# Performance work log

Measured on AMD Instinct MI355X. Metric: run time of the kernel, lower is better.

## Reference

```python
import jax, jax.numpy as jnp
import numpy as np

D_IN = 256
H = 512


def _linear_params(key, fan_in, fan_out):
    kw, kb = jax.random.split(key)
    bound = 1.0 / np.sqrt(fan_in)
    W = jax.random.uniform(kw, (fan_in, fan_out), minval=-bound, maxval=bound, dtype=jnp.float32)
    b = jax.random.uniform(kb, (fan_out,), minval=-bound, maxval=bound, dtype=jnp.float32)
    return W, b


def setup_inputs() -> dict:
    key = jax.random.key(0)
    ks = jax.random.split(key, 7)
    brick_vectors = jax.random.normal(ks[0], (8, 128, D_IN), dtype=jnp.float32)
    Wa, ba = _linear_params(ks[1], D_IN, H)
    Wb, bb = _linear_params(ks[2], H, H)
    Wca, bca = _linear_params(ks[3], 2 * H, H)
    Wcb, bcb = _linear_params(ks[4], H, H)
    Wcc, bcc = _linear_params(ks[5], H, H)
    Wo, bo = _linear_params(ks[6], H, 2)
    return {
        "brick_vectors": brick_vectors,
        "Wa": Wa, "ba": ba,
        "Wb": Wb, "bb": bb,
        "Wca": Wca, "bca": bca,
        "Wcb": Wcb, "bcb": bcb,
        "Wcc": Wcc, "bcc": bcc,
        "Wo": Wo, "bo": bo,
    }


def reference(brick_vectors, Wa, ba, Wb, bb, Wca, bca, Wcb, bcb, Wcc, bcc, Wo, bo):
    B, N, _ = brick_vectors.shape
    x = brick_vectors.reshape(-1, D_IN)            # [B*N, D_IN]
    f = jax.nn.relu(x @ Wa + ba)                   # node MLP
    f = jax.nn.relu(f @ Wb + bb)                   # [B*N, 512]
    f = f.reshape(B, N, H)
    # pairwise broadcast-concat: pair (i, j) gets cat(f[:, j], f[:, i])
    fa = jnp.broadcast_to(f[:, None, :, :], (B, N, N, H))   # varies over j (last pair axis)
    fb = jnp.broadcast_to(f[:, :, None, :], (B, N, N, H))   # varies over i
    e = jnp.concatenate((fa, fb), axis=-1).reshape(-1, 2 * H)  # [B*N*N, 1024]
    e = jax.nn.relu(e @ Wca + bca)
    e = jax.nn.relu(e @ Wcb + bcb)
    e = jax.nn.relu(e @ Wcc + bcc)
    out = e @ Wo + bo                               # [B*N*N, 2]
    return out.reshape(B, N, N, 2)
```

## Files before the change

### kernel.cpp

```cpp
#include <hip/hip_runtime.h>

typedef __bf16 bf16x8 __attribute__((ext_vector_type(8)));
typedef float f32x16 __attribute__((ext_vector_type(16)));

#define GLOAD_LDS16(gsrc, ldst)                                                   \
  __builtin_amdgcn_global_load_lds(                                               \
      (const __attribute__((address_space(1))) void*)(gsrc),                      \
      (__attribute__((address_space(3))) void*)(ldst), 16, 0, 0)

__device__ __forceinline__ void pack_one(const float* __restrict__ src,
                                         __bf16* __restrict__ dst,
                                         int t, int kbshift) {
  int e = t & 7, l = (t >> 3) & 63;
  int kb = (t >> 9) & ((1 << kbshift) - 1);
  int c = t >> (9 + kbshift);
  int k = kb * 16 + ((l >> 5) << 3) + e;
  int n = (c << 5) + (l & 31);
  dst[t] = (__bf16)src[k * 512 + n];
}

__global__ __launch_bounds__(256) void pack_all(
    const float* __restrict__ Wcb, const float* __restrict__ Wcc,
    const float* __restrict__ Wb, const float* __restrict__ Wca,
    const float* __restrict__ Wa,
    __bf16* __restrict__ Pb, __bf16* __restrict__ Pc,
    __bf16* __restrict__ PWb, __bf16* __restrict__ PH0,
    __bf16* __restrict__ PH1, __bf16* __restrict__ PWa) {
  int idx = blockIdx.x * 256 + threadIdx.x;
  if (idx < 262144) {
    pack_one(Wcb, Pb, idx, 5);
  } else if (idx < 524288) {
    pack_one(Wcc, Pc, idx - 262144, 5);
  } else if (idx < 786432) {
    pack_one(Wb, PWb, idx - 524288, 5);
  } else if (idx < 1048576) {
    pack_one(Wca, PH0, idx - 786432, 5);
  } else if (idx < 1310720) {
    pack_one(Wca + 512 * 512, PH1, idx - 1048576, 5);
  } else if (idx < 1441792) {
    pack_one(Wa, PWa, idx - 1310720, 4);
  }
}

template <int K>
__global__ __launch_bounds__(512, 2) void node_mfma(
    const float* __restrict__ A, const bf16x8* __restrict__ P0,
    const bf16x8* __restrict__ P1, const float* __restrict__ bias,
    int do_relu, float* __restrict__ C0, float* __restrict__ C1) {
  constexpr int KB = K / 16;
  constexpr int KH = K / 2;
  __shared__ __align__(16) char sA[64 * K * 2];

  int row0 = blockIdx.x * 64;
  const bf16x8* P = blockIdx.y ? P1 : P0;
  float* C = blockIdx.y ? C1 : C0;
  int tid = threadIdx.x, lane = tid & 63, w = tid >> 6;

  {
    int k2 = tid & (KH - 1);
    int rof = tid / KH;
    constexpr int RPI = 512 / KH;
#pragma unroll 4
    for (int it = 0; it < 64 / RPI; it++) {
      int r = it * RPI + rof;
      float2 aa = *(const float2*)(A + (row0 + r) * K + 2 * k2);
      unsigned short s0 = __builtin_bit_cast(unsigned short, (__bf16)aa.x);
      unsigned short s1 = __builtin_bit_cast(unsigned short, (__bf16)aa.y);
      unsigned int pk = ((unsigned int)s1 << 16) | (unsigned int)s0;
      int wbyte = r * (2 * K) + ((4 * k2) ^ ((r & 15) << 4));
      *(unsigned int*)(sA + wbyte) = pk;
    }
  }
  __syncthreads();

  int mrow = (w & 1) * 32;
  int n0 = (w >> 1) * 128;
  int cg4 = (w >> 1) * 4;
  int arow = mrow + (lane & 31);
  int sAk = (arow & 15) << 4;
  int klo = (lane >> 5) * 8;

  const bf16x8* B0 = P + ((cg4 + 0) * KB) * 64 + lane;
  const bf16x8* B1 = P + ((cg4 + 1) * KB) * 64 + lane;
  const bf16x8* B2 = P + ((cg4 + 2) * KB) * 64 + lane;
  const bf16x8* B3 = P + ((cg4 + 3) * KB) * 64 + lane;

  f32x16 acc[4];
#pragma unroll
  for (int nb = 0; nb < 4; nb++)
#pragma unroll
    for (int r = 0; r < 16; r++) acc[nb][r] = 0.f;

#pragma unroll 2
  for (int kb = 0; kb < KB; kb++) {
    int abyte = arow * (2 * K) + (((kb * 16 + klo) * 2) ^ sAk);
    bf16x8 a = *(const bf16x8*)(sA + abyte);
    bf16x8 b0 = B0[kb * 64];
    bf16x8 b1 = B1[kb * 64];
    bf16x8 b2 = B2[kb * 64];
    bf16x8 b3 = B3[kb * 64];
    acc[0] = __builtin_amdgcn_mfma_f32_32x32x16_bf16(a, b0, acc[0], 0, 0, 0);
    acc[1] = __builtin_amdgcn_mfma_f32_32x32x16_bf16(a, b1, acc[1], 0, 0, 0);
    acc[2] = __builtin_amdgcn_mfma_f32_32x32x16_bf16(a, b2, acc[2], 0, 0, 0);
    acc[3] = __builtin_amdgcn_mfma_f32_32x32x16_bf16(a, b3, acc[3], 0, 0, 0);
  }

#pragma unroll
  for (int nb = 0; nb < 4; nb++) {
    int cn = n0 + nb * 32 + (lane & 31);
    float bv = bias ? bias[cn] : 0.f;
#pragma unroll
    for (int r = 0; r < 16; r++) {
      int rr = mrow + (r & 3) + 8 * (r >> 2) + 4 * (lane >> 5);
      float val = acc[nb][r] + bv;
      if (do_relu) val = fmaxf(val, 0.f);
      C[(row0 + rr) * 512 + cn] = val;
    }
  }
}

__global__ __launch_bounds__(512, 2) void edge_kernel(
    const float* __restrict__ u, const float* __restrict__ v,
    const bf16x8* __restrict__ Pb, const bf16x8* __restrict__ Pc,
    const float* __restrict__ bca, const float* __restrict__ bcb,
    const float* __restrict__ bcc, const float* __restrict__ Wo,
    const float* __restrict__ bo, float* __restrict__ out) {
  __shared__ __align__(16) char h_raw[163840];
  char* Bst = h_raw + 131072;

  int wg = blockIdx.x;
  int i = wg & 127, b = wg >> 7;
  int tid = threadIdx.x, lane = tid & 63, w = tid >> 6;

  int mrow = (w & 1) * 32;
  int n0 = (w >> 1) * 128;
  int cg4 = (w >> 1) * 4;
  int arow = mrow + (lane & 31);
  int sA = (arow & 15) << 4;
  int klo = (lane >> 5) * 8;
  int cb0 = 2 * w;

#define STAGE_B(P, kb, sel)                                                       \
  {                                                                               \
    const char* _g0 = (const char*)((P) + (cb0 * 32 + (kb)) * 64) + lane * 16;    \
    const char* _g1 = (const char*)((P) + ((cb0 + 1) * 32 + (kb)) * 64) + lane * 16; \
    GLOAD_LDS16(_g0, Bst + (sel) * 16384 + cb0 * 1024);                           \
    GLOAD_LDS16(_g1, Bst + (sel) * 16384 + (cb0 + 1) * 1024);                     \
  }

  STAGE_B(Pb, 0, 0)

  {
    int k2 = tid & 255;
    float2 vv = *(const float2*)(v + (b * 128 + i) * 512 + 2 * k2);
    float2 bc = *(const float2*)(bca + 2 * k2);
    float vb0 = vv.x + bc.x, vb1 = vv.y + bc.y;
    const float* ub = u + (b * 128) * 512;
#pragma unroll 4
    for (int it = 0; it < 64; it++) {
      int r = it * 2 + (tid >> 8);
      float2 uu = *(const float2*)(ub + r * 512 + 2 * k2);
      float x0 = fmaxf(uu.x + vb0, 0.f);
      float x1 = fmaxf(uu.y + vb1, 0.f);
      unsigned short s0 = __builtin_bit_cast(unsigned short, (__bf16)x0);
      unsigned short s1 = __builtin_bit_cast(unsigned short, (__bf16)x1);
      unsigned int pk = ((unsigned int)s1 << 16) | (unsigned int)s0;
      int rt = r & 63;
      int wbyte = ((r >> 6) << 16) + rt * 1024 + ((4 * k2) ^ ((rt & 15) << 4));
      *(unsigned int*)(h_raw + wbyte) = pk;
    }
  }
  __syncthreads();

  f32x16 acc0[4], acc1[4];

#pragma unroll
  for (int nb = 0; nb < 4; nb++)
#pragma unroll
    for (int r = 0; r < 16; r++) { acc0[nb][r] = 0.f; acc1[nb][r] = 0.f; }
#pragma unroll 2
  for (int kb = 0; kb < 32; kb++) {
    int sel = kb & 1;
    if (kb < 31) STAGE_B(Pb, kb + 1, sel ^ 1)
    const char* bb = Bst + sel * 16384 + lane * 16;
    bf16x8 b0 = *(const bf16x8*)(bb + (cg4 + 0) * 1024);
    bf16x8 b1 = *(const bf16x8*)(bb + (cg4 + 1) * 1024);
    bf16x8 b2 = *(const bf16x8*)(bb + (cg4 + 2) * 1024);
    bf16x8 b3 = *(const bf16x8*)(bb + (cg4 + 3) * 1024);
    int abyte = arow * 1024 + (((kb * 16 + klo) * 2) ^ sA);
    bf16x8 a0 = *(const bf16x8*)(h_raw + abyte);
    bf16x8 a1 = *(const bf16x8*)(h_raw + 65536 + abyte);
    acc0[0] = __builtin_amdgcn_mfma_f32_32x32x16_bf16(a0, b0, acc0[0], 0, 0, 0);
    acc1[0] = __builtin_amdgcn_mfma_f32_32x32x16_bf16(a1, b0, acc1[0], 0, 0, 0);
    acc0[1] = __builtin_amdgcn_mfma_f32_32x32x16_bf16(a0, b1, acc0[1], 0, 0, 0);
    acc1[1] = __builtin_amdgcn_mfma_f32_32x32x16_bf16(a1, b1, acc1[1], 0, 0, 0);
    acc0[2] = __builtin_amdgcn_mfma_f32_32x32x16_bf16(a0, b2, acc0[2], 0, 0, 0);
    acc1[2] = __builtin_amdgcn_mfma_f32_32x32x16_bf16(a1, b2, acc1[2], 0, 0, 0);
    acc0[3] = __builtin_amdgcn_mfma_f32_32x32x16_bf16(a0, b3, acc0[3], 0, 0, 0);
    acc1[3] = __builtin_amdgcn_mfma_f32_32x32x16_bf16(a1, b3, acc1[3], 0, 0, 0);
    __syncthreads();
  }
  STAGE_B(Pc, 0, 0)

#pragma unroll
  for (int nb = 0; nb < 4; nb++) {
    int cn = n0 + nb * 32 + (lane & 31);
    float bbv = bcb[cn];
#pragma unroll
    for (int r = 0; r < 16; r++) {
      int row = mrow + (r & 3) + 8 * (r >> 2) + 4 * (lane >> 5);
      int byte_ = row * 1024 + ((cn * 2) ^ ((row & 15) << 4));
      *(__bf16*)(h_raw + byte_) = (__bf16)fmaxf(acc0[nb][r] + bbv, 0.f);
      *(__bf16*)(h_raw + 65536 + byte_) = (__bf16)fmaxf(acc1[nb][r] + bbv, 0.f);
    }
  }
  __syncthreads();

#pragma unroll
  for (int nb = 0; nb < 4; nb++)
#pragma unroll
    for (int r = 0; r < 16; r++) { acc0[nb][r] = 0.f; acc1[nb][r] = 0.f; }
#pragma unroll 2
  for (int kb = 0; kb < 32; kb++) {
    int sel = kb & 1;
    if (kb < 31) STAGE_B(Pc, kb + 1, sel ^ 1)
    const char* bb = Bst + sel * 16384 + lane * 16;
    bf16x8 b0 = *(const bf16x8*)(bb + (cg4 + 0) * 1024);
    bf16x8 b1 = *(const bf16x8*)(bb + (cg4 + 1) * 1024);
    bf16x8 b2 = *(const bf16x8*)(bb + (cg4 + 2) * 1024);
    bf16x8 b3 = *(const bf16x8*)(bb + (cg4 + 3) * 1024);
    int abyte = arow * 1024 + (((kb * 16 + klo) * 2) ^ sA);
    bf16x8 a0 = *(const bf16x8*)(h_raw + abyte);
    bf16x8 a1 = *(const bf16x8*)(h_raw + 65536 + abyte);
    acc0[0] = __builtin_amdgcn_mfma_f32_32x32x16_bf16(a0, b0, acc0[0], 0, 0, 0);
    acc1[0] = __builtin_amdgcn_mfma_f32_32x32x16_bf16(a1, b0, acc1[0], 0, 0, 0);
    acc0[1] = __builtin_amdgcn_mfma_f32_32x32x16_bf16(a0, b1, acc0[1], 0, 0, 0);
    acc1[1] = __builtin_amdgcn_mfma_f32_32x32x16_bf16(a1, b1, acc1[1], 0, 0, 0);
    acc0[2] = __builtin_amdgcn_mfma_f32_32x32x16_bf16(a0, b2, acc0[2], 0, 0, 0);
    acc1[2] = __builtin_amdgcn_mfma_f32_32x32x16_bf16(a1, b2, acc1[2], 0, 0, 0);
    acc0[3] = __builtin_amdgcn_mfma_f32_32x32x16_bf16(a0, b3, acc0[3], 0, 0, 0);
    acc1[3] = __builtin_amdgcn_mfma_f32_32x32x16_bf16(a1, b3, acc1[3], 0, 0, 0);
    __syncthreads();
  }

  float p0[16][2] = {}, p1[16][2] = {};
#pragma unroll
  for (int nb = 0; nb < 4; nb++) {
    int cn = n0 + nb * 32 + (lane & 31);
    float bcv = bcc[cn];
    float2 wov = *(const float2*)(Wo + cn * 2);
#pragma unroll
    for (int r = 0; r < 16; r++) {
      float h30 = fmaxf(acc0[nb][r] + bcv, 0.f);
      float h31 = fmaxf(acc1[nb][r] + bcv, 0.f);
      p0[r][0] += h30 * wov.x; p0[r][1] += h30 * wov.y;
      p1[r][0] += h31 * wov.x; p1[r][1] += h31 * wov.y;
    }
  }
#pragma unroll
  for (int m = 1; m <= 16; m <<= 1) {
#pragma unroll
    for (int r = 0; r < 16; r++) {
      p0[r][0] += __shfl_xor(p0[r][0], m, 64);
      p0[r][1] += __shfl_xor(p0[r][1], m, 64);
      p1[r][0] += __shfl_xor(p1[r][0], m, 64);
      p1[r][1] += __shfl_xor(p1[r][1], m, 64);
    }
  }
  __syncthreads();
  float* red = (float*)h_raw;
  if ((lane & 31) == 0) {
    int hh = lane >> 5, cg = w >> 1;
#pragma unroll
    for (int r = 0; r < 16; r++) {
      int row = mrow + (r & 3) + 8 * (r >> 2) + 4 * hh;
      red[(cg * 128 + row) * 2 + 0] = p0[r][0];
      red[(cg * 128 + row) * 2 + 1] = p0[r][1];
      red[(cg * 128 + 64 + row) * 2 + 0] = p1[r][0];
      red[(cg * 128 + 64 + row) * 2 + 1] = p1[r][1];
    }
  }
  __syncthreads();
  if (tid < 256) {
    int row = tid >> 1, d = tid & 1;
    float s = red[(0 * 128 + row) * 2 + d] + red[(1 * 128 + row) * 2 + d] +
              red[(2 * 128 + row) * 2 + d] + red[(3 * 128 + row) * 2 + d] + bo[d];
    out[((b * 128 + i) * 128 + row) * 2 + d] = s;
  }
#undef STAGE_B
}

extern "C" void kernel_launch(void* const* d_in, const int* in_sizes, int n_in,
                              void* d_out, int out_size, void* d_ws, size_t ws_size,
                              hipStream_t stream) {
  const float* x   = (const float*)d_in[0];
  const float* Wa  = (const float*)d_in[1];
  const float* ba  = (const float*)d_in[2];
  const float* Wb  = (const float*)d_in[3];
  const float* bb  = (const float*)d_in[4];
  const float* Wca = (const float*)d_in[5];
  const float* bca = (const float*)d_in[6];
  const float* Wcb = (const float*)d_in[7];
  const float* bcb = (const float*)d_in[8];
  const float* Wcc = (const float*)d_in[9];
  const float* bcc = (const float*)d_in[10];
  const float* Wo  = (const float*)d_in[11];
  const float* bo  = (const float*)d_in[12];
  float* out = (float*)d_out;

  char* ws = (char*)d_ws;
  float* f1 = (float*)(ws);
  float* f  = (float*)(ws + (2u << 20));
  float* u  = (float*)(ws + (4u << 20));
  float* v  = (float*)(ws + (6u << 20));
  __bf16* Pb  = (__bf16*)(ws + (8u << 20));
  __bf16* Pc  = (__bf16*)(ws + (8u << 20) + (512u << 10));
  __bf16* PWb = (__bf16*)(ws + (9u << 20));
  __bf16* PH0 = (__bf16*)(ws + (9u << 20) + (512u << 10));
  __bf16* PH1 = (__bf16*)(ws + (10u << 20));
  __bf16* PWa = (__bf16*)(ws + (10u << 20) + (512u << 10));

  pack_all<<<5632, 256, 0, stream>>>(Wcb, Wcc, Wb, Wca, Wa,
                                     Pb, Pc, PWb, PH0, PH1, PWa);
  node_mfma<256><<<dim3(16, 1), 512, 0, stream>>>(
      x, (const bf16x8*)PWa, (const bf16x8*)PWa, ba, 1, f1, f1);
  node_mfma<512><<<dim3(16, 1), 512, 0, stream>>>(
      f1, (const bf16x8*)PWb, (const bf16x8*)PWb, bb, 1, f, f);
  node_mfma<512><<<dim3(16, 2), 512, 0, stream>>>(
      f, (const bf16x8*)PH0, (const bf16x8*)PH1, nullptr, 0, u, v);
  edge_kernel<<<1024, 512, 0, stream>>>(u, v, (const bf16x8*)Pb, (const bf16x8*)Pc,
                                        bca, bcb, bcc, Wo, bo, out);
}
```

Before: 231.2 us.

## Split edge tiles in half and use per-wave 4-stage barrier-free B pipeline

Each workgroup of the edge kernel now handles 64 j-rows instead of 128, so twice as many workgroups are launched and LDS use drops to 128KB. Each wave computes a 64x64 output tile and stages only its own weight columns. That lets the k-loop drop its per-step __syncthreads in favour of a 4-slot ring of global->LDS loads with explicit vmcnt waits. MFMA issue is also wrapped in s_setprio. The cost is that the weights Pb and Pc are streamed twice as often overall, and the final reduction now has more per-wave partials.

```diff
diff --git a/kernel.cpp b/kernel.cpp
--- a/kernel.cpp
+++ b/kernel.cpp
@@ -125,39 +125,53 @@
     const float* __restrict__ bca, const float* __restrict__ bcb,
     const float* __restrict__ bcc, const float* __restrict__ Wo,
     const float* __restrict__ bo, float* __restrict__ out) {
-  __shared__ __align__(16) char h_raw[163840];
-  char* Bst = h_raw + 131072;
+  __shared__ __align__(16) char h_raw[131072];
+  char* Bst = h_raw + 65536;
 
   int wg = blockIdx.x;
-  int i = wg & 127, b = wg >> 7;
+  int jh = wg & 1, i = (wg >> 1) & 127, b = wg >> 8;
+  int j0 = jh * 64;
   int tid = threadIdx.x, lane = tid & 63, w = tid >> 6;
 
-  int mrow = (w & 1) * 32;
-  int n0 = (w >> 1) * 128;
-  int cg4 = (w >> 1) * 4;
-  int arow = mrow + (lane & 31);
-  int sA = (arow & 15) << 4;
+  int cb0 = 2 * w;
+  int r0 = lane & 31;
+  int sA = (r0 & 15) << 4;
   int klo = (lane >> 5) * 8;
-  int cb0 = 2 * w;
-
-#define STAGE_B(P, kb, sel)                                                       \
+
+#define STAGE_B(P, kb, slot)                                                      \
   {                                                                               \
-    const char* _g0 = (const char*)((P) + (cb0 * 32 + (kb)) * 64) + lane * 16;    \
-    const char* _g1 = (const char*)((P) + ((cb0 + 1) * 32 + (kb)) * 64) + lane * 16; \
-    GLOAD_LDS16(_g0, Bst + (sel) * 16384 + cb0 * 1024);                           \
-    GLOAD_LDS16(_g1, Bst + (sel) * 16384 + (cb0 + 1) * 1024);                     \
-  }
-
-  STAGE_B(Pb, 0, 0)
+    const char* g0_ = (const char*)((P) + ((cb0) * 32 + (kb)) * 64) + lane * 16;  \
+    const char* g1_ = (const char*)((P) + ((cb0 + 1) * 32 + (kb)) * 64) + lane * 16; \
+    GLOAD_LDS16(g0_, Bst + (slot) * 16384 + (cb0) * 1024);                        \
+    GLOAD_LDS16(g1_, Bst + (slot) * 16384 + (cb0 + 1) * 1024);                    \
+  }
+
+#define KSTEP(P, kb, DO_STAGE, VMSTR)                                             \
+  {                                                                               \
+    if (DO_STAGE) STAGE_B(P, (kb) + 3, ((kb) + 3) & 3)                            \
+    asm volatile("s_waitcnt vmcnt(" VMSTR ")" ::: "memory");                      \
+    const char* bb_ = Bst + ((kb) & 3) * 16384 + lane * 16;                       \
+    bf16x8 b0 = *(const bf16x8*)(bb_ + cb0 * 1024);                               \
+    bf16x8 b1 = *(const bf16x8*)(bb_ + (cb0 + 1) * 1024);                         \
+    int ab_ = (((kb) * 16 + klo) * 2) ^ sA;                                       \
+    bf16x8 a0 = *(const bf16x8*)(h_raw + r0 * 1024 + ab_);                        \
+    bf16x8 a1 = *(const bf16x8*)(h_raw + (r0 + 32) * 1024 + ab_);                 \
+    __builtin_amdgcn_s_setprio(1);                                                \
+    accA0 = __builtin_amdgcn_mfma_f32_32x32x16_bf16(a0, b0, accA0, 0, 0, 0);      \
+    accA1 = __builtin_amdgcn_mfma_f32_32x32x16_bf16(a0, b1, accA1, 0, 0, 0);      \
+    accB0 = __builtin_amdgcn_mfma_f32_32x32x16_bf16(a1, b0, accB0, 0, 0, 0);      \
+    accB1 = __builtin_amdgcn_mfma_f32_32x32x16_bf16(a1, b1, accB1, 0, 0, 0);      \
+    __builtin_amdgcn_s_setprio(0);                                                \
+  }
 
   {
     int k2 = tid & 255;
     float2 vv = *(const float2*)(v + (b * 128 + i) * 512 + 2 * k2);
     float2 bc = *(const float2*)(bca + 2 * k2);
     float vb0 = vv.x + bc.x, vb1 = vv.y + bc.y;
-    const float* ub = u + (b * 128) * 512;
+    const float* ub = u + (b * 128 + j0) * 512;
 #pragma unroll 4
-    for (int it = 0; it < 64; it++) {
+    for (int it = 0; it < 32; it++) {
       int r = it * 2 + (tid >> 8);
       float2 uu = *(const float2*)(ub + r * 512 + 2 * k2);
       float x0 = fmaxf(uu.x + vb0, 0.f);
@@ -165,128 +179,104 @@
       unsigned short s0 = __builtin_bit_cast(unsigned short, (__bf16)x0);
       unsigned short s1 = __builtin_bit_cast(unsigned short, (__bf16)x1);
       unsigned int pk = ((unsigned int)s1 << 16) | (unsigned int)s0;
-      int rt = r & 63;
-      int wbyte = ((r >> 6) << 16) + rt * 1024 + ((4 * k2) ^ ((rt & 15) << 4));
+      int wbyte = r * 1024 + ((4 * k2) ^ ((r & 15) << 4));
       *(unsigned int*)(h_raw + wbyte) = pk;
     }
   }
-  __syncthreads();
-
-  f32x16 acc0[4], acc1[4];
-
-#pragma unroll
-  for (int nb = 0; nb < 4; nb++)
-#pragma unroll
-    for (int r = 0; r < 16; r++) { acc0[nb][r] = 0.f; acc1[nb][r] = 0.f; }
-#pragma unroll 2
-  for (int kb = 0; kb < 32; kb++) {
-    int sel = kb & 1;
-    if (kb < 31) STAGE_B(Pb, kb + 1, sel ^ 1)
-    const char* bb = Bst + sel * 16384 + lane * 16;
-    bf16x8 b0 = *(const bf16x8*)(bb + (cg4 + 0) * 1024);
-    bf16x8 b1 = *(const bf16x8*)(bb + (cg4 + 1) * 1024);
-    bf16x8 b2 = *(const bf16x8*)(bb + (cg4 + 2) * 1024);
-    bf16x8 b3 = *(const bf16x8*)(bb + (cg4 + 3) * 1024);
-    int abyte = arow * 1024 + (((kb * 16 + klo) * 2) ^ sA);
-    bf16x8 a0 = *(const bf16x8*)(h_raw + abyte);
-    bf16x8 a1 = *(const bf16x8*)(h_raw + 65536 + abyte);
-    acc0[0] = __builtin_amdgcn_mfma_f32_32x32x16_bf16(a0, b0, acc0[0], 0, 0, 0);
-    acc1[0] = __builtin_amdgcn_mfma_f32_32x32x16_bf16(a1, b0, acc1[0], 0, 0, 0);
-    acc0[1] = __builtin_amdgcn_mfma_f32_32x32x16_bf16(a0, b1, acc0[1], 0, 0, 0);
-    acc1[1] = __builtin_amdgcn_mfma_f32_32x32x16_bf16(a1, b1, acc1[1], 0, 0, 0);
-    acc0[2] = __builtin_amdgcn_mfma_f32_32x32x16_bf16(a0, b2, acc0[2], 0, 0, 0);
-    acc1[2] = __builtin_amdgcn_mfma_f32_32x32x16_bf16(a1, b2, acc1[2], 0, 0, 0);
-    acc0[3] = __builtin_amdgcn_mfma_f32_32x32x16_bf16(a0, b3, acc0[3], 0, 0, 0);
-    acc1[3] = __builtin_amdgcn_mfma_f32_32x32x16_bf16(a1, b3, acc1[3], 0, 0, 0);
-    __syncthreads();
-  }
+
+  f32x16 accA0, accA1, accB0, accB1;
+#pragma unroll
+  for (int r = 0; r < 16; r++) { accA0[r] = 0.f; accA1[r] = 0.f; accB0[r] = 0.f; accB1[r] = 0.f; }
+
+  STAGE_B(Pb, 0, 0)
+  STAGE_B(Pb, 1, 1)
+  STAGE_B(Pb, 2, 2)
+  asm volatile("s_waitcnt lgkmcnt(0)" ::: "memory");
+  __builtin_amdgcn_s_barrier();
+
+  for (int kb = 0; kb < 29; kb++) KSTEP(Pb, kb, 1, "6")
+  KSTEP(Pb, 29, 0, "4")
+  KSTEP(Pb, 30, 0, "2")
+  KSTEP(Pb, 31, 0, "0")
+
   STAGE_B(Pc, 0, 0)
-
-#pragma unroll
-  for (int nb = 0; nb < 4; nb++) {
-    int cn = n0 + nb * 32 + (lane & 31);
+  STAGE_B(Pc, 1, 1)
+  STAGE_B(Pc, 2, 2)
+  asm volatile("s_waitcnt lgkmcnt(0)" ::: "memory");
+  __builtin_amdgcn_s_barrier();
+
+#pragma unroll
+  for (int blk = 0; blk < 2; blk++) {
+    int cn = cb0 * 32 + blk * 32 + (lane & 31);
     float bbv = bcb[cn];
+    const f32x16& A0 = blk ? accA1 : accA0;
+    const f32x16& A1 = blk ? accB1 : accB0;
 #pragma unroll
     for (int r = 0; r < 16; r++) {
-      int row = mrow + (r & 3) + 8 * (r >> 2) + 4 * (lane >> 5);
-      int byte_ = row * 1024 + ((cn * 2) ^ ((row & 15) << 4));
-      *(__bf16*)(h_raw + byte_) = (__bf16)fmaxf(acc0[nb][r] + bbv, 0.f);
-      *(__bf16*)(h_raw + 65536 + byte_) = (__bf16)fmaxf(acc1[nb][r] + bbv, 0.f);
-    }
-  }
-  __syncthreads();
-
-#pragma unroll
-  for (int nb = 0; nb < 4; nb++)
-#pragma unroll
-    for (int r = 0; r < 16; r++) { acc0[nb][r] = 0.f; acc1[nb][r] = 0.f; }
-#pragma unroll 2
-  for (int kb = 0; kb < 32; kb++) {
-    int sel = kb & 1;
-    if (kb < 31) STAGE_B(Pc, kb + 1, sel ^ 1)
-    const char* bb = Bst + sel * 16384 + lane * 16;
-    bf16x8 b0 = *(const bf16x8*)(bb + (cg4 + 0) * 1024);
-    bf16x8 b1 = *(const bf16x8*)(bb + (cg4 + 1) * 1024);
-    bf16x8 b2 = *(const bf16x8*)(bb + (cg4 + 2) * 1024);
-    bf16x8 b3 = *(const bf16x8*)(bb + (cg4 + 3) * 1024);
-    int abyte = arow * 1024 + (((kb * 16 + klo) * 2) ^ sA);
-    bf16x8 a0 = *(const bf16x8*)(h_raw + abyte);
-    bf16x8 a1 = *(const bf16x8*)(h_raw + 65536 + abyte);
-    acc0[0] = __builtin_amdgcn_mfma_f32_32x32x16_bf16(a0, b0, acc0[0], 0, 0, 0);
-    acc1[0] = __builtin_amdgcn_mfma_f32_32x32x16_bf16(a1, b0, acc1[0], 0, 0, 0);
-    acc0[1] = __builtin_amdgcn_mfma_f32_32x32x16_bf16(a0, b1, acc0[1], 0, 0, 0);
-    acc1[1] = __builtin_amdgcn_mfma_f32_32x32x16_bf16(a1, b1, acc1[1], 0, 0, 0);
-    acc0[2] = __builtin_amdgcn_mfma_f32_32x32x16_bf16(a0, b2, acc0[2], 0, 0, 0);
-    acc1[2] = __builtin_amdgcn_mfma_f32_32x32x16_bf16(a1, b2, acc1[2], 0, 0, 0);
-    acc0[3] = __builtin_amdgcn_mfma_f32_32x32x16_bf16(a0, b3, acc0[3], 0, 0, 0);
-    acc1[3] = __builtin_amdgcn_mfma_f32_32x32x16_bf16(a1, b3, acc1[3], 0, 0, 0);
-    __syncthreads();
-  }
-
-  float p0[16][2] = {}, p1[16][2] = {};
-#pragma unroll
-  for (int nb = 0; nb < 4; nb++) {
-    int cn = n0 + nb * 32 + (lane & 31);
-    float bcv = bcc[cn];
-    float2 wov = *(const float2*)(Wo + cn * 2);
-#pragma unroll
-    for (int r = 0; r < 16; r++) {
-      float h30 = fmaxf(acc0[nb][r] + bcv, 0.f);
-      float h31 = fmaxf(acc1[nb][r] + bcv, 0.f);
-      p0[r][0] += h30 * wov.x; p0[r][1] += h30 * wov.y;
-      p1[r][0] += h31 * wov.x; p1[r][1] += h31 * wov.y;
-    }
-  }
-#pragma unroll
-  for (int m = 1; m <= 16; m <<= 1) {
-#pragma unroll
-    for (int r = 0; r < 16; r++) {
-      p0[r][0] += __shfl_xor(p0[r][0], m, 64);
-      p0[r][1] += __shfl_xor(p0[r][1], m, 64);
-      p1[r][0] += __shfl_xor(p1[r][0], m, 64);
-      p1[r][1] += __shfl_xor(p1[r][1], m, 64);
-    }
-  }
+      int crow = (r & 3) + 8 * (r >> 2) + 4 * (lane >> 5);
+      int byte_ = crow * 1024 + ((cn * 2) ^ ((crow & 15) << 4));
+      *(__bf16*)(h_raw + byte_) = (__bf16)fmaxf(A0[r] + bbv, 0.f);
+      *(__bf16*)(h_raw + byte_ + 32 * 1024) = (__bf16)fmaxf(A1[r] + bbv, 0.f);
+    }
+  }
+#pragma unroll
+  for (int r = 0; r < 16; r++) { accA0[r] = 0.f; accA1[r] = 0.f; accB0[r] = 0.f; accB1[r] = 0.f; }
+  asm volatile("s_waitcnt lgkmcnt(0)" ::: "memory");
+  __builtin_amdgcn_s_barrier();
+
+  for (int kb = 0; kb < 29; kb++) KSTEP(Pc, kb, 1, "6")
+  KSTEP(Pc, 29, 0, "4")
+  KSTEP(Pc, 30, 0, "2")
+  KSTEP(Pc, 31, 0, "0")
+
   __syncthreads();
   float* red = (float*)h_raw;
-  if ((lane & 31) == 0) {
-    int hh = lane >> 5, cg = w >> 1;
-#pragma unroll
-    for (int r = 0; r < 16; r++) {
-      int row = mrow + (r & 3) + 8 * (r >> 2) + 4 * hh;
-      red[(cg * 128 + row) * 2 + 0] = p0[r][0];
-      red[(cg * 128 + row) * 2 + 1] = p0[r][1];
-      red[(cg * 128 + 64 + row) * 2 + 0] = p1[r][0];
-      red[(cg * 128 + 64 + row) * 2 + 1] = p1[r][1];
+
+#pragma unroll
+  for (int rg = 0; rg < 2; rg++) {
+    float p[16][2];
+#pragma unroll
+    for (int r = 0; r < 16; r++) { p[r][0] = 0.f; p[r][1] = 0.f; }
+#pragma unroll
+    for (int blk = 0; blk < 2; blk++) {
+      int cn = cb0 * 32 + blk * 32 + (lane & 31);
+      float bcv = bcc[cn];
+      float2 wov = *(const float2*)(Wo + cn * 2);
+      const f32x16& A = rg ? (blk ? accB1 : accB0) : (blk ? accA1 : accA0);
+#pragma unroll
+      for (int r = 0; r < 16; r++) {
+        float h3 = fmaxf(A[r] + bcv, 0.f);
+        p[r][0] += h3 * wov.x;
+        p[r][1] += h3 * wov.y;
+      }
+    }
+#pragma unroll
+    for (int m = 1; m <= 16; m <<= 1) {
+#pragma unroll
+      for (int r = 0; r < 16; r++) {
+        p[r][0] += __shfl_xor(p[r][0], m, 64);
+        p[r][1] += __shfl_xor(p[r][1], m, 64);
+      }
+    }
+    if ((lane & 31) == 0) {
+      int hh = lane >> 5;
+#pragma unroll
+      for (int r = 0; r < 16; r++) {
+        int crow = (r & 3) + 8 * (r >> 2) + 4 * hh;
+        red[(w * 64 + rg * 32 + crow) * 2 + 0] = p[r][0];
+        red[(w * 64 + rg * 32 + crow) * 2 + 1] = p[r][1];
+      }
     }
   }
   __syncthreads();
-  if (tid < 256) {
+  if (tid < 128) {
     int row = tid >> 1, d = tid & 1;
-    float s = red[(0 * 128 + row) * 2 + d] + red[(1 * 128 + row) * 2 + d] +
-              red[(2 * 128 + row) * 2 + d] + red[(3 * 128 + row) * 2 + d] + bo[d];
-    out[((b * 128 + i) * 128 + row) * 2 + d] = s;
-  }
+    float s = bo[d];
+#pragma unroll
+    for (int ww = 0; ww < 8; ww++) s += red[(ww * 64 + row) * 2 + d];
+    out[(((b * 128 + i) * 128) + j0 + row) * 2 + d] = s;
+  }
+#undef KSTEP
 #undef STAGE_B
 }
 
@@ -328,6 +318,6 @@
       f1, (const bf16x8*)PWb, (const bf16x8*)PWb, bb, 1, f, f);
   node_mfma<512><<<dim3(16, 2), 512, 0, stream>>>(
       f, (const bf16x8*)PH0, (const bf16x8*)PH1, nullptr, 0, u, v);
-  edge_kernel<<<1024, 512, 0, stream>>>(u, v, (const bf16x8*)Pb, (const bf16x8*)Pc,
+  edge_kernel<<<2048, 512, 0, stream>>>(u, v, (const bf16x8*)Pb, (const bf16x8*)Pc,
                                         bca, bcb, bcc, Wo, bo, out);
 }
```

Result: slower. 265.6 us (+14.9%).
